# Optimization experiments

Measured on AMD Instinct MI355X. Metric: run time of the kernel, lower is better.

The kernel has to match this reference:

```python
import jax, jax.numpy as jnp
import numpy as np
import math

K = 8  # n_prototypes
SQRT_2_OVER_PI = 0.7978845608028654  # sqrt(2/pi)
EPS = 1e-12  # torch F.normalize eps


def _gelu(x):
    # tanh-approx GELU, matching the module's _gelu
    return 0.5 * x * (1.0 + jnp.tanh(SQRT_2_OVER_PI * (x + 0.044715 * x * x * x)))


def _l2norm(x, axis=-1):
    n = jnp.linalg.norm(x, axis=axis, keepdims=True)
    return x / jnp.maximum(n, EPS)


def setup_inputs() -> dict:
    key = jax.random.key(0)
    k1, k2 = jax.random.split(key)
    B, T, D = 8, 2048, 2048
    x = jax.random.normal(k1, (B, T, D), dtype=jnp.float32)
    # prototype bank as it exists after initialization: unit-norm rows
    protos = _l2norm(jax.random.normal(k2, (K, D), dtype=jnp.float32))
    log_tau = jnp.asarray(math.log(2.0), dtype=jnp.float32)
    log_gamma = jnp.asarray(math.log(2.0), dtype=jnp.float32)
    log_blend = jnp.asarray(math.log(0.3 / 0.7), dtype=jnp.float32)
    return {"x": x, "protos": protos, "log_tau": log_tau,
            "log_gamma": log_gamma, "log_blend": log_blend}


def reference(x, protos, log_tau, log_gamma, log_blend):
    # steady-state (self._ready == True) forward path
    tau = jnp.exp(log_tau)
    gamma = jnp.exp(log_gamma)
    alpha = jax.nn.sigmoid(log_blend)

    out = _gelu(x)                                  # [B,T,D]
    out_norm = _l2norm(out)                         # [B,T,D]
    proto_norm = _l2norm(protos)                    # [K,D]
    sims = jnp.einsum('btd,kd->btk', out_norm, proto_norm)  # [B,T,K]
    soft_max_sim = (jax.nn.logsumexp(sims * tau, axis=-1) / tau
                    - jnp.log(jnp.float32(K)) / tau)         # [B,T]
    novelty = jnp.exp(-gamma * soft_max_sim)
    gate = 1.0 - alpha + alpha * novelty            # [B,T]
    return out * gate[..., None]
```

## Files before the change

### kernel.cpp

```cpp
#include <hip/hip_runtime.h>
#include <math.h>

#define DDIM 2048
#define KP 8
#define BLOCK 256

typedef float f4 __attribute__((ext_vector_type(4)));

__device__ __forceinline__ unsigned short f32_to_bf16_rne(float f) {
    unsigned u = __float_as_uint(f);
    unsigned r = u + 0x7FFFu + ((u >> 16) & 1u);
    return (unsigned short)(r >> 16);
}

__device__ __forceinline__ float gelu_f(float x) {
    float x2 = x * x;
    float inner = x * fmaf(0.044715f, x2, 1.0f);
    float e = __expf(-1.5957691216057308f * inner);
    return x * __builtin_amdgcn_rcpf(1.0f + e);
}

__device__ __forceinline__ float wave_reduce_add(float v) {
#pragma unroll
    for (int m = 32; m >= 1; m >>= 1) v += __shfl_xor(v, m, 64);
    return v;
}

__global__ void proto_prep_kernel(const float* __restrict__ protos,
                                  unsigned short* __restrict__ pb,
                                  float* __restrict__ inv_pn) {
    const int k = blockIdx.x;
    const int tid = threadIdx.x;
    const float* p = protos + k * DDIM;
    float ss = 0.0f;
#pragma unroll
    for (int i = 0; i < 2; ++i) {
        int idx = tid + i * 256;
        f4 a = reinterpret_cast<const f4*>(p)[idx];
        ushort4 u;
        u.x = f32_to_bf16_rne(a.x); u.y = f32_to_bf16_rne(a.y);
        u.z = f32_to_bf16_rne(a.z); u.w = f32_to_bf16_rne(a.w);
        float q;
        q = __uint_as_float((unsigned)u.x << 16); ss += q * q;
        q = __uint_as_float((unsigned)u.y << 16); ss += q * q;
        q = __uint_as_float((unsigned)u.z << 16); ss += q * q;
        q = __uint_as_float((unsigned)u.w << 16); ss += q * q;
        *reinterpret_cast<ushort4*>(&pb[(size_t)k * DDIM + idx * 4]) = u;
    }
    ss = wave_reduce_add(ss);
    __shared__ float red[4];
    const int wave = tid >> 6, lane = tid & 63;
    if (lane == 0) red[wave] = ss;
    __syncthreads();
    if (tid == 0)
        inv_pn[k] = 1.0f / fmaxf(sqrtf(red[0] + red[1] + red[2] + red[3]), 1e-12f);
}

__global__ __launch_bounds__(BLOCK)
void fused_row_kernel(const float* __restrict__ x,
                      const unsigned short* __restrict__ pb,
                      const float* __restrict__ lt,
                      const float* __restrict__ lg,
                      const float* __restrict__ lb,
                      const float* __restrict__ inv_pn,
                      float* __restrict__ out, int nrows) {
    alignas(16) __shared__ float red[2][9][4];

    const int tid = threadIdx.x;
    const int lane = tid & 63;
    const int wave = tid >> 6;

    const float tau = __expf(lt[0]);
    const float gamma = __expf(lg[0]);
    const float alpha = 1.0f / (1.0f + __expf(-lb[0]));
    const float inv_tau = 1.0f / tau;
    const float logK_div_tau = logf(8.0f) * inv_tau;

    float ipn[KP];
#pragma unroll
    for (int k = 0; k < KP; ++k) ipn[k] = inv_pn[k];

    const uint2* pb2 = reinterpret_cast<const uint2*>(pb);

    int buf = 0;
    for (int row = blockIdx.x; row < nrows; row += gridDim.x) {
        const f4* xr = reinterpret_cast<const f4*>(x + (size_t)row * DDIM);
        f4 a = xr[tid];
        f4 b = xr[tid + 256];

        f4 ga, gb;
        ga.x = gelu_f(a.x); ga.y = gelu_f(a.y);
        ga.z = gelu_f(a.z); ga.w = gelu_f(a.w);
        gb.x = gelu_f(b.x); gb.y = gelu_f(b.y);
        gb.z = gelu_f(b.z); gb.w = gelu_f(b.w);

        float vals[9];
        vals[8] = ga.x * ga.x + ga.y * ga.y + ga.z * ga.z + ga.w * ga.w
                + gb.x * gb.x + gb.y * gb.y + gb.z * gb.z + gb.w * gb.w;

#pragma unroll
        for (int k = 0; k < KP; ++k) {
            uint2 p0 = pb2[k * 512 + tid];
            uint2 p1 = pb2[k * 512 + 256 + tid];
            float q0 = __uint_as_float(p0.x << 16);
            float q1 = __uint_as_float(p0.x & 0xFFFF0000u);
            float q2 = __uint_as_float(p0.y << 16);
            float q3 = __uint_as_float(p0.y & 0xFFFF0000u);
            float r0 = __uint_as_float(p1.x << 16);
            float r1 = __uint_as_float(p1.x & 0xFFFF0000u);
            float r2 = __uint_as_float(p1.y << 16);
            float r3 = __uint_as_float(p1.y & 0xFFFF0000u);
            float t;
            t = fmaf(q0, ga.x, q1 * ga.y);
            t = fmaf(q2, ga.z, t);
            t = fmaf(q3, ga.w, t);
            t = fmaf(r0, gb.x, t);
            t = fmaf(r1, gb.y, t);
            t = fmaf(r2, gb.z, t);
            t = fmaf(r3, gb.w, t);
            vals[k] = t;
        }

#pragma unroll
        for (int v = 0; v < 9; ++v) vals[v] = wave_reduce_add(vals[v]);

        if (lane == 0) {
#pragma unroll
            for (int v = 0; v < 9; ++v) red[buf][v][wave] = vals[v];
        }
        __syncthreads();

        float s[9];
#pragma unroll
        for (int v = 0; v < 9; ++v) {
            f4 r = *reinterpret_cast<const f4*>(red[buf][v]);
            s[v] = (r.x + r.y) + (r.z + r.w);
        }
        buf ^= 1;

        const float invn = 1.0f / fmaxf(sqrtf(s[8]), 1e-12f);
        float m = -1e30f;
        float z[KP];
#pragma unroll
        for (int k = 0; k < KP; ++k) {
            z[k] = s[k] * invn * ipn[k] * tau;
            m = fmaxf(m, z[k]);
        }
        float e = 0.0f;
#pragma unroll
        for (int k = 0; k < KP; ++k) e += __expf(z[k] - m);
        float lse = m + __logf(e);
        float sms = lse * inv_tau - logK_div_tau;
        float nov = __expf(-gamma * sms);
        const float gate = 1.0f - alpha + alpha * nov;

        f4* orow = reinterpret_cast<f4*>(out + (size_t)row * DDIM);
        f4 oa, ob;
        oa.x = ga.x * gate; oa.y = ga.y * gate;
        oa.z = ga.z * gate; oa.w = ga.w * gate;
        ob.x = gb.x * gate; ob.y = gb.y * gate;
        ob.z = gb.z * gate; ob.w = gb.w * gate;
        __builtin_nontemporal_store(oa, &orow[tid]);
        __builtin_nontemporal_store(ob, &orow[tid + 256]);
    }
}

extern "C" void kernel_launch(void* const* d_in, const int* in_sizes, int n_in,
                              void* d_out, int out_size, void* d_ws, size_t ws_size,
                              hipStream_t stream) {
    const float* x = (const float*)d_in[0];
    const float* protos = (const float*)d_in[1];
    const float* lt = (const float*)d_in[2];
    const float* lg = (const float*)d_in[3];
    const float* lb = (const float*)d_in[4];
    float* out = (float*)d_out;

    float* inv_pn = (float*)d_ws;
    unsigned short* pb = (unsigned short*)((char*)d_ws + 256);

    const int nrows = in_sizes[0] / DDIM;

    proto_prep_kernel<<<KP, 256, 0, stream>>>(protos, pb, inv_pn);

    int blocks = nrows < 4096 ? nrows : 4096;
    fused_row_kernel<<<blocks, BLOCK, 0, stream>>>(x, pb, lt, lg, lb, inv_pn,
                                                   out, nrows);
}
```

Before: 63.31 us.

## Prefetch next row of x and use bf16 dot2 for prototype similarities

```diff
diff --git a/kernel.cpp b/kernel.cpp
--- a/kernel.cpp
+++ b/kernel.cpp
@@ -6,6 +6,13 @@
 #define BLOCK 256
 
 typedef float f4 __attribute__((ext_vector_type(4)));
+
+#if __has_builtin(__builtin_amdgcn_fdot2_f32_bf16)
+#define HAVE_DOT2 1
+typedef __bf16 bf2 __attribute__((ext_vector_type(2)));
+#else
+#define HAVE_DOT2 0
+#endif
 
 __device__ __forceinline__ unsigned short f32_to_bf16_rne(float f) {
     unsigned u = __float_as_uint(f);
@@ -83,10 +90,22 @@
     const uint2* pb2 = reinterpret_cast<const uint2*>(pb);
 
     int buf = 0;
-    for (int row = blockIdx.x; row < nrows; row += gridDim.x) {
+    int row = blockIdx.x;
+    f4 a, b;
+    if (row < nrows) {
         const f4* xr = reinterpret_cast<const f4*>(x + (size_t)row * DDIM);
-        f4 a = xr[tid];
-        f4 b = xr[tid + 256];
+        a = xr[tid];
+        b = xr[tid + 256];
+    }
+
+    for (; row < nrows; row += gridDim.x) {
+        const int nxt = row + gridDim.x;
+        f4 na, nb;
+        if (nxt < nrows) {
+            const f4* xn = reinterpret_cast<const f4*>(x + (size_t)nxt * DDIM);
+            na = xn[tid];
+            nb = xn[tid + 256];
+        }
 
         f4 ga, gb;
         ga.x = gelu_f(a.x); ga.y = gelu_f(a.y);
@@ -98,6 +117,24 @@
         vals[8] = ga.x * ga.x + ga.y * ga.y + ga.z * ga.z + ga.w * ga.w
                 + gb.x * gb.x + gb.y * gb.y + gb.z * gb.z + gb.w * gb.w;
 
+#if HAVE_DOT2
+        bf2 gp0, gp1, gp2, gp3;
+        gp0.x = (__bf16)ga.x; gp0.y = (__bf16)ga.y;
+        gp1.x = (__bf16)ga.z; gp1.y = (__bf16)ga.w;
+        gp2.x = (__bf16)gb.x; gp2.y = (__bf16)gb.y;
+        gp3.x = (__bf16)gb.z; gp3.y = (__bf16)gb.w;
+#pragma unroll
+        for (int k = 0; k < KP; ++k) {
+            uint2 p0 = pb2[k * 512 + tid];
+            uint2 p1 = pb2[k * 512 + 256 + tid];
+            float t;
+            t = __builtin_amdgcn_fdot2_f32_bf16(gp0, __builtin_bit_cast(bf2, p0.x), 0.0f, false);
+            t = __builtin_amdgcn_fdot2_f32_bf16(gp1, __builtin_bit_cast(bf2, p0.y), t, false);
+            t = __builtin_amdgcn_fdot2_f32_bf16(gp2, __builtin_bit_cast(bf2, p1.x), t, false);
+            t = __builtin_amdgcn_fdot2_f32_bf16(gp3, __builtin_bit_cast(bf2, p1.y), t, false);
+            vals[k] = t;
+        }
+#else
 #pragma unroll
         for (int k = 0; k < KP; ++k) {
             uint2 p0 = pb2[k * 512 + tid];
@@ -120,6 +157,7 @@
             t = fmaf(r3, gb.w, t);
             vals[k] = t;
         }
+#endif
 
 #pragma unroll
         for (int v = 0; v < 9; ++v) vals[v] = wave_reduce_add(vals[v]);
@@ -162,6 +200,9 @@
         ob.z = gb.z * gate; ob.w = gb.w * gate;
         __builtin_nontemporal_store(oa, &orow[tid]);
         __builtin_nontemporal_store(ob, &orow[tid + 256]);
+
+        a = na;
+        b = nb;
     }
 }
 
```

Measured after the change: 60.48 us. 4.5% less time.
